# Kernel tuning notes

Measured on AMD Instinct MI355X. Metric: run time of the kernel, lower is better.

Reference implementation:

```python
import jax, jax.numpy as jnp
import numpy as np

EPS = 1e-5

def bn_relu(y, g, b):
    # BatchNorm1d in training mode: stats over (B, L) per channel, biased variance
    mu = jnp.mean(y, axis=(0, 2), keepdims=True)
    var = jnp.var(y, axis=(0, 2), keepdims=True)
    yn = (y - mu) * jax.lax.rsqrt(var + EPS)
    return jax.nn.relu(yn * g[None, :, None] + b[None, :, None])

def conv1x1_pad1(x, W):
    # Conv1d(k=1, padding=1, bias=False): pointwise matmul then zero-pad length by 1 each side
    y = jnp.einsum('bcl,oc->bol', x, W)
    return jnp.pad(y, ((0, 0), (0, 0), (1, 1)))

def conv1x1(x, W, b):
    return jnp.einsum('bcl,oc->bol', x, W) + b[None, :, None]

def conv3_pad1(x, W):
    # Conv1d(k=3, padding=1, bias=False); W: [O, C, 3]
    return jax.lax.conv_general_dilated(x, W, window_strides=(1,), padding=((1, 1),),
                                        dimension_numbers=('NCH', 'OIH', 'NCH'))

def pam(f, Wq, bq, Wk, bk, Wv, bv, gamma):
    q = conv1x1(f, Wq, bq)          # [B, C//8, L]
    k = conv1x1(f, Wk, bk)          # [B, C//8, L]
    v = conv1x1(f, Wv, bv)          # [B, C, L]
    energy = jnp.einsum('bql,bqm->blm', q, k)   # [B, L, L]
    attn = jax.nn.softmax(energy, axis=-1)
    out = jnp.einsum('bcm,blm->bcl', v, attn)
    return gamma * out + f

def cam(f, gamma):
    energy = jnp.einsum('bcl,bdl->bcd', f, f)    # [B, C, C]
    energy_new = jnp.max(energy, axis=-1, keepdims=True) - energy
    attn = jax.nn.softmax(energy_new, axis=-1)
    out = jnp.einsum('bcd,bdl->bcl', attn, f)
    return gamma * out + f

def setup_inputs() -> dict:
    key = jax.random.key(0)
    ks = jax.random.split(key, 24)
    B, C, L = 8, 256, 2046
    IC, OC = C // 4, 128  # inter_channels=64, out_channels
    s = 0.05
    d = {
        'x':   jax.random.normal(ks[0], (B, C, L), jnp.float32),
        'W5a': jax.random.normal(ks[1], (IC, C), jnp.float32) * s,
        'g5a': jnp.ones((IC,), jnp.float32), 'b5a': jnp.zeros((IC,), jnp.float32),
        'W5c': jax.random.normal(ks[2], (IC, C), jnp.float32) * s,
        'g5c': jnp.ones((IC,), jnp.float32), 'b5c': jnp.zeros((IC,), jnp.float32),
        'Wq':  jax.random.normal(ks[3], (IC // 8, IC), jnp.float32) * s,
        'bq':  jnp.zeros((IC // 8,), jnp.float32),
        'Wk':  jax.random.normal(ks[4], (IC // 8, IC), jnp.float32) * s,
        'bk':  jnp.zeros((IC // 8,), jnp.float32),
        'Wv':  jax.random.normal(ks[5], (IC, IC), jnp.float32) * s,
        'bv':  jnp.zeros((IC,), jnp.float32),
        'gamma_pam': jnp.full((1,), 0.1, jnp.float32),
        'gamma_cam': jnp.full((1,), 0.1, jnp.float32),
        'W51': jax.random.normal(ks[6], (IC, IC, 3), jnp.float32) * s,
        'g51': jnp.ones((IC,), jnp.float32), 'b51': jnp.zeros((IC,), jnp.float32),
        'W52': jax.random.normal(ks[7], (IC, IC, 3), jnp.float32) * s,
        'g52': jnp.ones((IC,), jnp.float32), 'b52': jnp.zeros((IC,), jnp.float32),
        'W6':  jax.random.normal(ks[8], (OC, IC), jnp.float32) * s,
        'b6':  jnp.zeros((OC,), jnp.float32),
        'W7':  jax.random.normal(ks[9], (OC, IC), jnp.float32) * s,
        'b7':  jnp.zeros((OC,), jnp.float32),
        'W8':  jax.random.normal(ks[10], (OC, IC), jnp.float32) * s,
        'b8':  jnp.zeros((OC,), jnp.float32),
    }
    return d

def reference(x, W5a, g5a, b5a, W5c, g5c, b5c, Wq, bq, Wk, bk, Wv, bv,
              gamma_pam, gamma_cam, W51, g51, b51, W52, g52, b52,
              W6, b6, W7, b7, W8, b8):
    # dropout (p=0.1) treated as identity (eval mode)
    feat1 = bn_relu(conv1x1_pad1(x, W5a), g5a, b5a)          # [B, IC, L+2]
    sa_feat = pam(feat1, Wq, bq, Wk, bk, Wv, bv, gamma_pam)
    sa_conv = bn_relu(conv3_pad1(sa_feat, W51), g51, b51)
    sa_output = conv1x1(sa_conv, W6, b6)                     # [B, OC, L+2]
    feat2 = bn_relu(conv1x1_pad1(x, W5c), g5c, b5c)
    sc_feat = cam(feat2, gamma_cam)
    sc_conv = bn_relu(conv3_pad1(sc_feat, W52), g52, b52)
    sc_output = conv1x1(sc_conv, W7, b7)
    feat_sum = sa_conv + sc_conv
    sasc = conv1x1(feat_sum, W8, b8)
    # pool == 'maxpool' selects AdaptiveAvgPool1d(1) in the original (note swap)
    sasc = jnp.mean(sasc, axis=-1)                            # [B, OC]
    return (sasc, sa_output, sc_output)
```

## Files before the change

### kernel.cpp

```cpp
#include <hip/hip_runtime.h>
#include <math.h>

#define B 8
#define C 256
#define L 2046
#define LP 2048
#define IC 64
#define OC 128
#define BN_EPS 1e-5f
#define INVN (1.f / 16384.f)

#define OFF_Y1T    0u
#define OFF_Y2C    524288u
#define OFF_SAFT   1048576u
#define OFF_SCFT   1572864u
#define OFF_Y51T   2097152u
#define OFF_Y52T   2621440u
#define OFF_VB     3145728u
#define OFF_QT     3670016u
#define OFF_KT     3735552u
#define OFF_LPART  3801088u
#define OFF_EPART  3866624u
#define OFF_ATTN   4390912u
#define OFF_PART1  4423680u
#define OFF_PART2  4489216u
#define OFF_COEF1  4554752u
#define OFF_COEF2  4555008u
#define OFF_FSUM   4555264u
#define OFF_W5BF   4555776u
#define OFF_W67    4572160u
#define OFF_WT     4580352u
#define OFF_WQKV   4592640u
#define OFF_BQKV   4595200u

typedef __attribute__((ext_vector_type(8))) short bshort8;
typedef __attribute__((ext_vector_type(4))) float f32x4;

__device__ __forceinline__ unsigned short f2bf(float f) {
    union { float f; unsigned int u; } v; v.f = f;
    unsigned int r = v.u + 0x7fffu + ((v.u >> 16) & 1u);
    return (unsigned short)(r >> 16);
}
__device__ __forceinline__ float bf2f(unsigned short u) {
    union { unsigned int i; float f; } v; v.i = ((unsigned int)u) << 16;
    return v.f;
}
__device__ __forceinline__ unsigned int pk2(float a, float b) {
    return (unsigned int)f2bf(a) | ((unsigned int)f2bf(b) << 16);
}

__global__ __launch_bounds__(256) void k_wprep(
        const float* __restrict__ W5a, const float* __restrict__ W5c,
        const float* __restrict__ W6, const float* __restrict__ W7,
        const float* __restrict__ W51, const float* __restrict__ W52,
        const float* __restrict__ Wq, const float* __restrict__ Wk,
        const float* __restrict__ Wv, const float* __restrict__ bq,
        const float* __restrict__ bk, const float* __restrict__ bv,
        unsigned short* __restrict__ W5BF, unsigned short* __restrict__ W67,
        unsigned short* __restrict__ WT, unsigned short* __restrict__ WQKV,
        float* __restrict__ BQKV, float* __restrict__ FSUM) {
    int i = blockIdx.x * 256 + threadIdx.x;
    if (i < 32768) {
        int o = i >> 8, c = i & 255;
        W5BF[i] = f2bf(o < 64 ? W5a[o * 256 + c] : W5c[(o - 64) * 256 + c]);
    } else if (i < 49152) {
        int j = i - 32768; int g = j >> 13; int r = j & 8191;
        W67[j] = f2bf(g ? W7[r] : W6[r]);
    } else if (i < 73728) {
        int j = i - 49152;
        int c = j & 63, o = (j >> 6) & 63, wt = j >> 12; int w = wt / 3, t = wt % 3;
        const float* Ws = w ? W52 : W51;
        WT[j] = f2bf(Ws[(o * 64 + c) * 3 + t]);
    } else if (i < 78848) {
        int j = i - 73728; int o = j >> 6, c = j & 63;
        float v = o < 8 ? Wq[o * 64 + c] : (o < 16 ? Wk[(o - 8) * 64 + c] : Wv[(o - 16) * 64 + c]);
        WQKV[j] = f2bf(v);
    } else if (i < 78928) {
        int o = i - 78848;
        BQKV[o] = o < 8 ? bq[o] : (o < 16 ? bk[o - 8] : bv[o - 16]);
    } else if (i < 79440) {
        FSUM[i - 78928] = 0.f;
    }
}

__global__ __launch_bounds__(256) void k_conv1(const float* __restrict__ x,
        const unsigned short* __restrict__ W5BF,
        unsigned short* __restrict__ Y1T, unsigned short* __restrict__ Y2C,
        float* __restrict__ PART1) {
    __shared__ float lds_part[4][128];
    int lt = blockIdx.x, og = blockIdx.y, b = blockIdx.z;
    int w = threadIdx.x >> 6, lane = threadIdx.x & 63;
    int n = lane & 15, quad = lane >> 4;
    int lp = lt * 64 + w * 16 + n;
    int ls = lp - 1;
    bool valid = (ls >= 0) && (ls < L);
    f32x4 acc[4];
#pragma unroll
    for (int ot = 0; ot < 4; ++ot) acc[ot] = (f32x4){0.f, 0.f, 0.f, 0.f};
    for (int ck = 0; ck < 8; ++ck) {
        int c0 = ck * 32 + quad * 8;
        bshort8 xb = {};
        if (valid) {
            const float* xs = x + ((size_t)(b * C + c0)) * L + ls;
#pragma unroll
            for (int j = 0; j < 8; ++j)
                ((unsigned short*)&xb)[j] = f2bf(xs[(size_t)j * L]);
        }
#pragma unroll
        for (int ot = 0; ot < 4; ++ot) {
            bshort8 wf = *(const bshort8*)(W5BF + (size_t)(og * 64 + ot * 16 + n) * C + ck * 32 + quad * 8);
            acc[ot] = __builtin_amdgcn_mfma_f32_16x16x32_bf16(wf, xb, acc[ot], 0, 0, 0);
        }
    }
    if (og == 0) {
#pragma unroll
        for (int ot = 0; ot < 4; ++ot) {
            uint2 pv;
            pv.x = pk2(acc[ot][0], acc[ot][1]);
            pv.y = pk2(acc[ot][2], acc[ot][3]);
            *(uint2*)(Y1T + ((size_t)(b * LP + lp)) * IC + ot * 16 + quad * 4) = pv;
        }
    } else {
#pragma unroll
        for (int ot = 0; ot < 4; ++ot)
#pragma unroll
            for (int r = 0; r < 4; ++r) {
                int o = ot * 16 + quad * 4 + r;
                Y2C[((size_t)(b * IC + o)) * LP + lp] = f2bf(acc[ot][r]);
            }
    }
#pragma unroll
    for (int ot = 0; ot < 4; ++ot)
#pragma unroll
        for (int r = 0; r < 4; ++r) {
            float s = acc[ot][r], q = s * s;
#pragma unroll
            for (int msk = 1; msk < 16; msk <<= 1) {
                s += __shfl_xor(s, msk, 64);
                q += __shfl_xor(q, msk, 64);
            }
            if (n == 0) {
                int ch = ot * 16 + quad * 4 + r;
                lds_part[w][ch * 2] = s;
                lds_part[w][ch * 2 + 1] = q;
            }
        }
    __syncthreads();
    int t = threadIdx.x;
    if (t < 128) {
        float s = lds_part[0][t] + lds_part[1][t] + lds_part[2][t] + lds_part[3][t];
        PART1[(size_t)(og * 128 + t) * 256 + (b * 32 + lt)] = s;
    }
}

__global__ __launch_bounds__(256) void k_red(const float* __restrict__ PART,
        const float* __restrict__ g0, const float* __restrict__ b0,
        const float* __restrict__ g1, const float* __restrict__ b1,
        float* __restrict__ COEF) {
    int ch = blockIdx.x;
    int t = threadIdx.x;
    float s = PART[(size_t)(ch * 2) * 256 + t];
    float q = PART[(size_t)(ch * 2 + 1) * 256 + t];
    for (int off = 32; off; off >>= 1) {
        s += __shfl_down(s, off, 64);
        q += __shfl_down(q, off, 64);
    }
    __shared__ float rs[4], rq[4];
    if ((t & 63) == 0) { rs[t >> 6] = s; rq[t >> 6] = q; }
    __syncthreads();
    if (t == 0) {
        float S = rs[0] + rs[1] + rs[2] + rs[3];
        float Q = rq[0] + rq[1] + rq[2] + rq[3];
        float mu = S * INVN;
        float var = Q * INVN - mu * mu;
        float gv = ch < 64 ? g0[ch] : g1[ch - 64];
        float bv = ch < 64 ? b0[ch] : b1[ch - 64];
        float A = gv * rsqrtf(var + BN_EPS);
        COEF[ch * 2] = A;
        COEF[ch * 2 + 1] = bv - mu * A;
    }
}

__global__ __launch_bounds__(256) void k_qkv(const unsigned short* __restrict__ Y1T,
        const float* __restrict__ COEF1,
        const unsigned short* __restrict__ WQKV, const float* __restrict__ BQKV,
        unsigned short* __restrict__ QT, unsigned short* __restrict__ KT,
        unsigned short* __restrict__ VB) {
    __shared__ float cA[64], cB[64];
    int lt = blockIdx.x, b = blockIdx.y;
    int t = threadIdx.x;
    if (t < 64) { cA[t] = COEF1[t * 2]; cB[t] = COEF1[t * 2 + 1]; }
    __syncthreads();
    int w = t >> 6, lane = t & 63, n = lane & 15, quad = lane >> 4;
    int lrow = lt * 64 + w * 16 + n;
    bshort8 fb[2];
#pragma unroll
    for (int kt = 0; kt < 2; ++kt) {
        bshort8 raw = *(const bshort8*)(Y1T + ((size_t)(b * LP + lrow)) * IC + kt * 32 + quad * 8);
        bshort8 f;
#pragma unroll
        for (int j = 0; j < 8; ++j) {
            int c = kt * 32 + quad * 8 + j;
            float v = fmaf(cA[c], bf2f((unsigned short)raw[j]), cB[c]);
            v = fmaxf(v, 0.f);
            ((unsigned short*)&f)[j] = f2bf(v);
        }
        fb[kt] = f;
    }
    f32x4 acc[5];
#pragma unroll
    for (int ot = 0; ot < 5; ++ot) {
        f32x4 a = {0.f, 0.f, 0.f, 0.f};
#pragma unroll
        for (int kt = 0; kt < 2; ++kt) {
            bshort8 wf = *(const bshort8*)(WQKV + (size_t)(ot * 16 + n) * IC + kt * 32 + quad * 8);
            a = __builtin_amdgcn_mfma_f32_16x16x32_bf16(wf, fb[kt], a, 0, 0, 0);
        }
        acc[ot] = a;
    }
#pragma unroll
    for (int ot = 0; ot < 5; ++ot)
#pragma unroll
        for (int r = 0; r < 4; ++r) {
            int o = ot * 16 + quad * 4 + r;
            unsigned short bv16 = f2bf(acc[ot][r] + BQKV[o]);
            if (ot == 0) {
                if (o < 8) QT[((size_t)(b * LP + lrow)) * 8 + o] = bv16;
                else KT[((size_t)(b * LP + lrow)) * 8 + (o - 8)] = bv16;
            } else {
                VB[((size_t)(b * IC + (o - 16))) * LP + lrow] = bv16;
            }
        }
}

__global__ __launch_bounds__(256) void k_pam(
        const unsigned short* __restrict__ qT, const unsigned short* __restrict__ kT,
        const unsigned short* __restrict__ vb,
        unsigned short* __restrict__ OPART, float* __restrict__ LPART) {
    __shared__ unsigned char smem[18432];
    unsigned short* vs = (unsigned short*)smem;
    unsigned short* ps = vs + 4608;
    float* os = (float*)smem;
    int qt = blockIdx.x, ks = blockIdx.y, b = blockIdx.z;
    int l0 = qt * 64;
    int tid = threadIdx.x;
    int wq = tid >> 6, lane = tid & 63, n = lane & 15, quad = lane >> 4;
    bshort8 qa = {};
    if (quad == 0)
        qa = *(const bshort8*)(qT + ((size_t)(b * LP + l0 + wq * 16 + n)) * 8);
    f32x4 acc[4];
#pragma unroll
    for (int s = 0; s < 4; ++s) acc[s] = (f32x4){0.f, 0.f, 0.f, 0.f};
    float li[4] = {0.f, 0.f, 0.f, 0.f};
    unsigned short* pw = ps + wq * 16 * 72;

    for (int it = 0; it < 8; ++it) {
        int m0 = ks * 512 + it * 64;
        __syncthreads();
        {
            int row = tid >> 2, chn = tid & 3;
            const unsigned short* src = vb + ((size_t)(b * IC + row)) * LP + m0 + chn * 16;
            unsigned short* dstl = vs + row * 72 + chn * 16;
            *(bshort8*)dstl = *(const bshort8*)src;
            *(bshort8*)(dstl + 8) = *(const bshort8*)(src + 8);
        }
        bshort8 kb[4];
#pragma unroll
        for (int s = 0; s < 4; ++s) kb[s] = (bshort8){};
        if (quad == 0) {
#pragma unroll
            for (int s = 0; s < 4; ++s)
                kb[s] = *(const bshort8*)(kT + ((size_t)(b * LP + m0 + s * 16 + n)) * 8);
        }
        __syncthreads();
        f32x4 sc[4];
#pragma unroll
        for (int s = 0; s < 4; ++s)
            sc[s] = __builtin_amdgcn_mfma_f32_16x16x32_bf16(qa, kb[s],
                        (f32x4){0.f, 0.f, 0.f, 0.f}, 0, 0, 0);
#pragma unroll
        for (int s = 0; s < 4; ++s)
#pragma unroll
            for (int r = 0; r < 4; ++r) {
                float p = __expf(sc[s][r]);
                li[r] += p;
                pw[(quad * 4 + r) * 72 + s * 16 + n] = f2bf(p);
            }
#pragma unroll
        for (int step = 0; step < 2; ++step) {
            bshort8 pa = *(const bshort8*)(pw + n * 72 + step * 32 + quad * 8);
#pragma unroll
            for (int s = 0; s < 4; ++s) {
                bshort8 vf = *(const bshort8*)(vs + (s * 16 + n) * 72 + step * 32 + quad * 8);
                acc[s] = __builtin_amdgcn_mfma_f32_16x16x32_bf16(pa, vf, acc[s], 0, 0, 0);
            }
        }
    }
    __syncthreads();
#pragma unroll
    for (int s = 0; s < 4; ++s)
#pragma unroll
        for (int r = 0; r < 4; ++r)
            os[(s * 16 + n) * 65 + wq * 16 + quad * 4 + r] = acc[s][r];
    size_t lbase = ((size_t)((b * 32 + qt) * 4 + ks)) * 64;
#pragma unroll
    for (int r = 0; r < 4; ++r) {
        float s_ = li[r];
#pragma unroll
        for (int msk = 1; msk < 16; msk <<= 1) s_ += __shfl_xor(s_, msk, 64);
        if (n == 0) LPART[lbase + wq * 16 + quad * 4 + r] = s_;
    }
    __syncthreads();
    size_t ob = ((size_t)((b * 32 + qt) * 4 + ks)) * 4096;
    int c = tid >> 2, qc = tid & 3;
    unsigned int* od = (unsigned int*)(OPART + ob + c * 64 + qc * 16);
#pragma unroll
    for (int i = 0; i < 8; ++i)
        od[i] = pk2(os[c * 65 + qc * 16 + 2 * i], os[c * 65 + qc * 16 + 2 * i + 1]);
}

__global__ __launch_bounds__(256) void k_pam_combine(
        const unsigned short* __restrict__ OPART, const float* __restrict__ LPART,
        const unsigned short* __restrict__ Y1T, const float* __restrict__ COEF1,
        const float* __restrict__ gamma, unsigned short* __restrict__ SAFT) {
    __shared__ float dn[64];
    __shared__ float cA[64], cB[64];
    __shared__ unsigned short tile[64 * 66];
    int qt = blockIdx.x, b = blockIdx.y;
    int l0 = qt * 64;
    int t = threadIdx.x;
    if (t < 64) {
        cA[t] = COEF1[t * 2]; cB[t] = COEF1[t * 2 + 1];
        size_t lbase = ((size_t)((b * 32 + qt) * 4)) * 64;
        dn[t] = LPART[lbase + t] + LPART[lbase + 64 + t] +
                LPART[lbase + 128 + t] + LPART[lbase + 192 + t];
    }
    __syncthreads();
    int c = t >> 2, qc = t & 3;
    float O[16];
#pragma unroll
    for (int i = 0; i < 16; ++i) O[i] = 0.f;
    size_t ob = ((size_t)((b * 32 + qt) * 4)) * 4096 + c * 64 + qc * 16;
#pragma unroll
    for (int s = 0; s < 4; ++s) {
        bshort8 p0 = *(const bshort8*)(OPART + ob + (size_t)s * 4096);
        bshort8 p1 = *(const bshort8*)(OPART + ob + (size_t)s * 4096 + 8);
#pragma unroll
        for (int i = 0; i < 8; ++i) {
            O[i]     += bf2f((unsigned short)p0[i]);
            O[8 + i] += bf2f((unsigned short)p1[i]);
        }
    }
    float gm = gamma[0];
#pragma unroll
    for (int i = 0; i < 16; ++i) {
        int q = qc * 16 + i;
        unsigned short raw = Y1T[((size_t)(b * LP + l0 + q)) * IC + c];
        float f1v = fmaxf(fmaf(cA[c], bf2f(raw), cB[c]), 0.f);
        float val = fmaf(gm, O[i] / dn[q], f1v);
        tile[q * 66 + c] = f2bf(val);
    }
    __syncthreads();
    int li = t >> 2, cc = t & 3;
    unsigned int* dst = (unsigned int*)(SAFT + ((size_t)(b * LP + l0 + li)) * IC + cc * 16);
#pragma unroll
    for (int i = 0; i < 8; ++i)
        dst[i] = *(unsigned int*)(tile + li * 66 + cc * 16 + 2 * i);
}

__global__ __launch_bounds__(256) void k_gram(const unsigned short* __restrict__ Y2C,
        const float* __restrict__ COEF1, float* __restrict__ EPART) {
    __shared__ float fs[64][132];
    __shared__ float cA[64], cB[64];
    int b = blockIdx.y;
    int l0 = blockIdx.x * 128;
    int t = threadIdx.x;
    if (t < 64) { cA[t] = COEF1[(64 + t) * 2]; cB[t] = COEF1[(64 + t) * 2 + 1]; }
    __syncthreads();
    for (int i = t; i < 64 * 64; i += 256) {
        int c = i >> 6, i2 = i & 63;
        unsigned int u = *(const unsigned int*)(Y2C + ((size_t)(b * IC + c)) * LP + l0 + i2 * 2);
        float A = cA[c], Bc = cB[c];
        fs[c][i2 * 2]     = fmaxf(fmaf(A, bf2f((unsigned short)u), Bc), 0.f);
        fs[c][i2 * 2 + 1] = fmaxf(fmaf(A, bf2f((unsigned short)(u >> 16)), Bc), 0.f);
    }
    __syncthreads();
    int c = t >> 2, dg = t & 3;
    float acc[16];
#pragma unroll
    for (int i = 0; i < 16; ++i) acc[i] = 0.f;
    for (int i4 = 0; i4 < 32; ++i4) {
        const float4 fc = *reinterpret_cast<const float4*>(&fs[c][i4 * 4]);
#pragma unroll
        for (int dd = 0; dd < 16; ++dd) {
            const float4 fd = *reinterpret_cast<const float4*>(&fs[dg * 16 + dd][i4 * 4]);
            acc[dd] += fc.x * fd.x + fc.y * fd.y + fc.z * fd.z + fc.w * fd.w;
        }
    }
    size_t base = ((size_t)(b * 16 + blockIdx.x)) * 4096 + c * 64 + dg * 16;
    for (int dd = 0; dd < 16; ++dd)
        EPART[base + dd] = acc[dd];
}

__global__ __launch_bounds__(256) void k_cam_softmax(const float* __restrict__ EPART,
        float* __restrict__ attn) {
    __shared__ float e[4096];
    int b = blockIdx.x, t = threadIdx.x;
    for (int idx = t; idx < 4096; idx += 256) {
        float s = 0.f;
        for (int ch = 0; ch < 16; ++ch) s += EPART[((size_t)(b * 16 + ch)) * 4096 + idx];
        e[idx] = s;
    }
    __syncthreads();
    if (t < 64) {
        float mn = INFINITY;
        for (int d = 0; d < 64; ++d) mn = fminf(mn, e[t * 64 + d]);
        float s = 0.f;
        float* a = attn + (size_t)b * 4096 + t * 64;
        for (int d = 0; d < 64; ++d) { float p = __expf(mn - e[t * 64 + d]); a[d] = p; s += p; }
        float inv = 1.f / s;
        for (int d = 0; d < 64; ++d) a[d] *= inv;
    }
}

__global__ __launch_bounds__(256) void k_cam_apply(const float* __restrict__ attn,
        const unsigned short* __restrict__ Y2C, const float* __restrict__ COEF1,
        const float* __restrict__ gamma, unsigned short* __restrict__ SCFT) {
    __shared__ __align__(16) float as[64 * 64];
    __shared__ float cA[64], cB[64];
    __shared__ unsigned short tile[128 * 66];
    int b = blockIdx.y;
    int l0 = blockIdx.x * 128;
    int t = threadIdx.x;
    int lq = t & 127, ch = t >> 7;
    if (t < 64) { cA[t] = COEF1[(64 + t) * 2]; cB[t] = COEF1[(64 + t) * 2 + 1]; }
    for (int i = t; i < 4096; i += 256) as[i] = attn[(size_t)b * 4096 + i];
    __syncthreads();
    float acc[32];
#pragma unroll
    for (int i = 0; i < 32; ++i) acc[i] = 0.f;
    const unsigned short* fb = Y2C + (size_t)b * IC * LP + l0 + lq;
    for (int d4 = 0; d4 < 16; ++d4) {
        float fv[4];
#pragma unroll
        for (int i = 0; i < 4; ++i) {
            int d = 4 * d4 + i;
            fv[i] = fmaxf(fmaf(cA[d], bf2f(fb[(size_t)d * LP]), cB[d]), 0.f);
        }
#pragma unroll
        for (int cc = 0; cc < 32; ++cc) {
            const float4 a4 = *reinterpret_cast<const float4*>(as + (ch * 32 + cc) * 64 + d4 * 4);
            acc[cc] += a4.x * fv[0] + a4.y * fv[1] + a4.z * fv[2] + a4.w * fv[3];
        }
    }
    float gm = gamma[0];
#pragma unroll
    for (int cc = 0; cc < 32; ++cc) {
        int c = ch * 32 + cc;
        float res = fmaxf(fmaf(cA[c], bf2f(fb[(size_t)c * LP]), cB[c]), 0.f);
        tile[lq * 66 + c] = f2bf(fmaf(gm, acc[cc], res));
    }
    __syncthreads();
    int li = t >> 1, half = t & 1;
    unsigned int* dst = (unsigned int*)(SCFT + ((size_t)(b * LP + l0 + li)) * IC + half * 32);
#pragma unroll
    for (int i = 0; i < 16; ++i)
        dst[i] = *(unsigned int*)(tile + li * 66 + half * 32 + 2 * i);
}

__global__ __launch_bounds__(256) void k_conv3(const unsigned short* __restrict__ SAFT,
        const unsigned short* __restrict__ SCFT, const unsigned short* __restrict__ WTall,
        unsigned short* __restrict__ Y51T, unsigned short* __restrict__ Y52T,
        float* __restrict__ PART2) {
    __shared__ float lds_part[4][128];
    int lt = blockIdx.x, og = blockIdx.y, b = blockIdx.z;
    const unsigned short* FTsrc = og ? SCFT : SAFT;
    const unsigned short* WT = WTall + og * 12288;
    unsigned short* dst = og ? Y52T : Y51T;
    int l0 = lt * 64;
    int w = threadIdx.x >> 6, lane = threadIdx.x & 63, n = lane & 15, quad = lane >> 4;
    int lrow = l0 + w * 16 + n;
    f32x4 acc[4];
#pragma unroll
    for (int ot = 0; ot < 4; ++ot) acc[ot] = (f32x4){0.f, 0.f, 0.f, 0.f};
#pragma unroll
    for (int t3 = 0; t3 < 3; ++t3) {
        int row = lrow + t3 - 1;
        bshort8 fb[2];
#pragma unroll
        for (int kt = 0; kt < 2; ++kt) {
            if (row >= 0 && row < LP)
                fb[kt] = *(const bshort8*)(FTsrc + ((size_t)(b * LP + row)) * IC + kt * 32 + quad * 8);
            else fb[kt] = (bshort8){};
        }
#pragma unroll
        for (int ot = 0; ot < 4; ++ot)
#pragma unroll
            for (int kt = 0; kt < 2; ++kt) {
                bshort8 wf = *(const bshort8*)(WT + ((size_t)(t3 * 64 + ot * 16 + n)) * IC + kt * 32 + quad * 8);
                acc[ot] = __builtin_amdgcn_mfma_f32_16x16x32_bf16(wf, fb[kt], acc[ot], 0, 0, 0);
            }
    }
#pragma unroll
    for (int ot = 0; ot < 4; ++ot) {
        uint2 pv;
        pv.x = pk2(acc[ot][0], acc[ot][1]);
        pv.y = pk2(acc[ot][2], acc[ot][3]);
        *(uint2*)(dst + ((size_t)(b * LP + lrow)) * IC + ot * 16 + quad * 4) = pv;
    }
#pragma unroll
    for (int ot = 0; ot < 4; ++ot)
#pragma unroll
        for (int r = 0; r < 4; ++r) {
            float s = acc[ot][r], q = s * s;
#pragma unroll
            for (int msk = 1; msk < 16; msk <<= 1) {
                s += __shfl_xor(s, msk, 64);
                q += __shfl_xor(q, msk, 64);
            }
            if (n == 0) {
                int cch = ot * 16 + quad * 4 + r;
                lds_part[w][cch * 2] = s;
                lds_part[w][cch * 2 + 1] = q;
            }
        }
    __syncthreads();
    int t = threadIdx.x;
    if (t < 128) {
        float s = lds_part[0][t] + lds_part[1][t] + lds_part[2][t] + lds_part[3][t];
        PART2[(size_t)(og * 128 + t) * 256 + (b * 32 + lt)] = s;
    }
}

__global__ __launch_bounds__(256) void k_final(const unsigned short* __restrict__ Y51T,
        const unsigned short* __restrict__ Y52T, const float* __restrict__ COEF2,
        const unsigned short* __restrict__ W67,
        const float* __restrict__ b6, const float* __restrict__ b7,
        float* __restrict__ out_sa, float* __restrict__ out_sc,
        float* __restrict__ FSUM) {
    __shared__ float cA[128], cB[128];
    __shared__ float fsw[4][64];
    int lt = blockIdx.x, og = blockIdx.y, b = blockIdx.z;
    int t = threadIdx.x;
    if (t < 128) { cA[t] = COEF2[t * 2]; cB[t] = COEF2[t * 2 + 1]; }
    __syncthreads();
    int w = t >> 6, lane = t & 63, n = lane & 15, quad = lane >> 4;
    int lrow = lt * 64 + w * 16 + n;
    float fs_lane[16];
    bshort8 ba[2], bb[2];
#pragma unroll
    for (int kt = 0; kt < 2; ++kt) {
        bshort8 ra = *(const bshort8*)(Y51T + ((size_t)(b * LP + lrow)) * IC + kt * 32 + quad * 8);
        bshort8 rb = *(const bshort8*)(Y52T + ((size_t)(b * LP + lrow)) * IC + kt * 32 + quad * 8);
        bshort8 fa, fb;
#pragma unroll
        for (int j = 0; j < 8; ++j) {
            int c = kt * 32 + quad * 8 + j;
            float v1 = fmaxf(fmaf(cA[c], bf2f((unsigned short)ra[j]), cB[c]), 0.f);
            float v2 = fmaxf(fmaf(cA[64 + c], bf2f((unsigned short)rb[j]), cB[64 + c]), 0.f);
            ((unsigned short*)&fa)[j] = f2bf(v1);
            ((unsigned short*)&fb)[j] = f2bf(v2);
            fs_lane[kt * 8 + j] = v1 + v2;
        }
        ba[kt] = fa; bb[kt] = fb;
    }
    f32x4 accA[4], accB[4];
#pragma unroll
    for (int ot = 0; ot < 4; ++ot) {
        accA[ot] = (f32x4){0.f, 0.f, 0.f, 0.f};
        accB[ot] = (f32x4){0.f, 0.f, 0.f, 0.f};
    }
#pragma unroll
    for (int ot = 0; ot < 4; ++ot)
#pragma unroll
        for (int kt = 0; kt < 2; ++kt) {
            bshort8 wa = *(const bshort8*)(W67 + (size_t)(og * 64 + ot * 16 + n) * IC + kt * 32 + quad * 8);
            bshort8 wb = *(const bshort8*)(W67 + 8192 + (size_t)(og * 64 + ot * 16 + n) * IC + kt * 32 + quad * 8);
            accA[ot] = __builtin_amdgcn_mfma_f32_16x16x32_bf16(wa, ba[kt], accA[ot], 0, 0, 0);
            accB[ot] = __builtin_amdgcn_mfma_f32_16x16x32_bf16(wb, bb[kt], accB[ot], 0, 0, 0);
        }
#pragma unroll
    for (int ot = 0; ot < 4; ++ot)
#pragma unroll
        for (int r = 0; r < 4; ++r) {
            int o = og * 64 + ot * 16 + quad * 4 + r;
            out_sa[((size_t)(b * OC + o)) * LP + lrow] = accA[ot][r] + b6[o];
            out_sc[((size_t)(b * OC + o)) * LP + lrow] = accB[ot][r] + b7[o];
        }
    if (og == 0) {
#pragma unroll
        for (int i = 0; i < 16; ++i) {
            float s = fs_lane[i];
#pragma unroll
            for (int msk = 1; msk < 16; msk <<= 1) s += __shfl_xor(s, msk, 64);
            if (n == 0) {
                int c = (i >> 3) * 32 + quad * 8 + (i & 7);
                fsw[w][c] = s;
            }
        }
        __syncthreads();
        if (t < 64)
            atomicAdd(&FSUM[b * 64 + t], fsw[0][t] + fsw[1][t] + fsw[2][t] + fsw[3][t]);
    }
}

__global__ __launch_bounds__(128) void k_sasc(const float* __restrict__ FSUM,
        const float* __restrict__ W8, const float* __restrict__ b8,
        float* __restrict__ out) {
    __shared__ float mean[64];
    int b = blockIdx.x, t = threadIdx.x;
    if (t < 64) mean[t] = FSUM[b * 64 + t] * (1.f / (float)LP);
    __syncthreads();
    float s = b8[t];
    for (int c = 0; c < 64; ++c) s = fmaf(W8[t * 64 + c], mean[c], s);
    out[b * OC + t] = s;
}

extern "C" void kernel_launch(void* const* d_in, const int* in_sizes, int n_in,
                              void* d_out, int out_size, void* d_ws, size_t ws_size,
                              hipStream_t stream) {
    (void)in_sizes; (void)n_in; (void)out_size; (void)ws_size;
    const float* x    = (const float*)d_in[0];
    const float* W5a  = (const float*)d_in[1];
    const float* g5a  = (const float*)d_in[2];
    const float* b5a  = (const float*)d_in[3];
    const float* W5c  = (const float*)d_in[4];
    const float* g5c  = (const float*)d_in[5];
    const float* b5c  = (const float*)d_in[6];
    const float* Wq   = (const float*)d_in[7];
    const float* bq   = (const float*)d_in[8];
    const float* Wk   = (const float*)d_in[9];
    const float* bk   = (const float*)d_in[10];
    const float* Wv   = (const float*)d_in[11];
    const float* bv   = (const float*)d_in[12];
    const float* gpam = (const float*)d_in[13];
    const float* gcam = (const float*)d_in[14];
    const float* W51  = (const float*)d_in[15];
    const float* g51  = (const float*)d_in[16];
    const float* b51  = (const float*)d_in[17];
    const float* W52  = (const float*)d_in[18];
    const float* g52  = (const float*)d_in[19];
    const float* b52  = (const float*)d_in[20];
    const float* W6   = (const float*)d_in[21];
    const float* b6   = (const float*)d_in[22];
    const float* W7   = (const float*)d_in[23];
    const float* b7   = (const float*)d_in[24];
    const float* W8   = (const float*)d_in[25];
    const float* b8   = (const float*)d_in[26];

    float* ws = (float*)d_ws;
    float* out = (float*)d_out;
    unsigned short* Y1T  = (unsigned short*)(ws + OFF_Y1T);
    unsigned short* Y2C  = (unsigned short*)(ws + OFF_Y2C);
    unsigned short* SAFT = (unsigned short*)(ws + OFF_SAFT);
    unsigned short* SCFT = (unsigned short*)(ws + OFF_SCFT);
    unsigned short* Y51T = (unsigned short*)(ws + OFF_Y51T);
    unsigned short* Y52T = (unsigned short*)(ws + OFF_Y52T);
    unsigned short* VB   = (unsigned short*)(ws + OFF_VB);
    unsigned short* QT   = (unsigned short*)(ws + OFF_QT);
    unsigned short* KT   = (unsigned short*)(ws + OFF_KT);
    float* LPART  = ws + OFF_LPART;
    float* EPART  = ws + OFF_EPART;
    float* ATTN   = ws + OFF_ATTN;
    float* PART1  = ws + OFF_PART1;
    float* PART2  = ws + OFF_PART2;
    float* COEF1  = ws + OFF_COEF1;
    float* COEF2  = ws + OFF_COEF2;
    float* FSUM   = ws + OFF_FSUM;
    unsigned short* W5BF = (unsigned short*)(ws + OFF_W5BF);
    unsigned short* W67  = (unsigned short*)(ws + OFF_W67);
    unsigned short* WT   = (unsigned short*)(ws + OFF_WT);
    unsigned short* WQKV = (unsigned short*)(ws + OFF_WQKV);
    float* BQKV = ws + OFF_BQKV;

    float* out_sa = out + B * OC;
    float* out_sc = out + B * OC + (size_t)B * OC * LP;
    unsigned short* OPART = (unsigned short*)out_sa;

    k_wprep<<<311, 256, 0, stream>>>(W5a, W5c, W6, W7, W51, W52, Wq, Wk, Wv,
                                     bq, bk, bv, W5BF, W67, WT, WQKV, BQKV, FSUM);
    k_conv1<<<dim3(32, 2, B), 256, 0, stream>>>(x, W5BF, Y1T, Y2C, PART1);
    k_red<<<128, 256, 0, stream>>>(PART1, g5a, b5a, g5c, b5c, COEF1);
    k_qkv<<<dim3(32, B), 256, 0, stream>>>(Y1T, COEF1, WQKV, BQKV, QT, KT, VB);
    k_pam<<<dim3(32, 4, B), 256, 0, stream>>>(QT, KT, VB, OPART, LPART);
    k_pam_combine<<<dim3(32, B), 256, 0, stream>>>(OPART, LPART, Y1T, COEF1, gpam, SAFT);
    k_gram<<<dim3(16, B), 256, 0, stream>>>(Y2C, COEF1, EPART);
    k_cam_softmax<<<B, 256, 0, stream>>>(EPART, ATTN);
    k_cam_apply<<<dim3(16, B), 256, 0, stream>>>(ATTN, Y2C, COEF1, gcam, SCFT);
    k_conv3<<<dim3(32, 2, B), 256, 0, stream>>>(SAFT, SCFT, WT, Y51T, Y52T, PART2);
    k_red<<<128, 256, 0, stream>>>(PART2, g51, b51, g52, b52, COEF2);
    k_final<<<dim3(32, 2, B), 256, 0, stream>>>(Y51T, Y52T, COEF2, W67, b6, b7,
                                                out_sa, out_sc, FSUM);
    k_sasc<<<B, 128, 0, stream>>>(FSUM, W8, b8, out);
}
```

Measured before the change: 243.4 us.

## Merge conv1 output groups per block and move CAM gram to bf16 MFMA

k_conv1 now computes all 128 output channels (both branches) in one block, loading and converting each x tile to bf16 once instead of twice. The launch grid halves and each block does twice the MFMA work. k_gram replaces the fp32 LDS dot-product loop with bf16 MFMA, producing 64 per-wave partial gram matrices per batch that k_cam_softmax then sums, so the workspace offsets grow. This lowers gram compute cost and x reads, but lowers gram precision to bf16 and raises the partial-sum traffic in the softmax kernel.

```diff
diff --git a/kernel.cpp b/kernel.cpp
--- a/kernel.cpp
+++ b/kernel.cpp
@@ -21,17 +21,17 @@
 #define OFF_KT     3735552u
 #define OFF_LPART  3801088u
 #define OFF_EPART  3866624u
-#define OFF_ATTN   4390912u
-#define OFF_PART1  4423680u
-#define OFF_PART2  4489216u
-#define OFF_COEF1  4554752u
-#define OFF_COEF2  4555008u
-#define OFF_FSUM   4555264u
-#define OFF_W5BF   4555776u
-#define OFF_W67    4572160u
-#define OFF_WT     4580352u
-#define OFF_WQKV   4592640u
-#define OFF_BQKV   4595200u
+#define OFF_ATTN   5963776u
+#define OFF_PART1  5996544u
+#define OFF_PART2  6062080u
+#define OFF_COEF1  6127616u
+#define OFF_COEF2  6127872u
+#define OFF_FSUM   6128128u
+#define OFF_W5BF   6128640u
+#define OFF_W67    6145024u
+#define OFF_WT     6153216u
+#define OFF_WQKV   6165504u
+#define OFF_BQKV   6168064u
 
 typedef __attribute__((ext_vector_type(8))) short bshort8;
 typedef __attribute__((ext_vector_type(4))) float f32x4;
@@ -87,50 +87,52 @@
         const unsigned short* __restrict__ W5BF,
         unsigned short* __restrict__ Y1T, unsigned short* __restrict__ Y2C,
         float* __restrict__ PART1) {
-    __shared__ float lds_part[4][128];
-    int lt = blockIdx.x, og = blockIdx.y, b = blockIdx.z;
+    __shared__ float lds_part[4][256];
+    int lt = blockIdx.x, b = blockIdx.y;
     int w = threadIdx.x >> 6, lane = threadIdx.x & 63;
     int n = lane & 15, quad = lane >> 4;
     int lp = lt * 64 + w * 16 + n;
     int ls = lp - 1;
     bool valid = (ls >= 0) && (ls < L);
-    f32x4 acc[4];
-#pragma unroll
-    for (int ot = 0; ot < 4; ++ot) acc[ot] = (f32x4){0.f, 0.f, 0.f, 0.f};
+    bshort8 xb[8];
+#pragma unroll
     for (int ck = 0; ck < 8; ++ck) {
-        int c0 = ck * 32 + quad * 8;
-        bshort8 xb = {};
+        bshort8 v = {};
         if (valid) {
-            const float* xs = x + ((size_t)(b * C + c0)) * L + ls;
+            const float* xs = x + ((size_t)(b * C + ck * 32 + quad * 8)) * L + ls;
 #pragma unroll
             for (int j = 0; j < 8; ++j)
-                ((unsigned short*)&xb)[j] = f2bf(xs[(size_t)j * L]);
-        }
-#pragma unroll
-        for (int ot = 0; ot < 4; ++ot) {
-            bshort8 wf = *(const bshort8*)(W5BF + (size_t)(og * 64 + ot * 16 + n) * C + ck * 32 + quad * 8);
-            acc[ot] = __builtin_amdgcn_mfma_f32_16x16x32_bf16(wf, xb, acc[ot], 0, 0, 0);
-        }
-    }
-    if (og == 0) {
-#pragma unroll
-        for (int ot = 0; ot < 4; ++ot) {
-            uint2 pv;
-            pv.x = pk2(acc[ot][0], acc[ot][1]);
-            pv.y = pk2(acc[ot][2], acc[ot][3]);
-            *(uint2*)(Y1T + ((size_t)(b * LP + lp)) * IC + ot * 16 + quad * 4) = pv;
-        }
-    } else {
-#pragma unroll
-        for (int ot = 0; ot < 4; ++ot)
-#pragma unroll
-            for (int r = 0; r < 4; ++r) {
-                int o = ot * 16 + quad * 4 + r;
-                Y2C[((size_t)(b * IC + o)) * LP + lp] = f2bf(acc[ot][r]);
-            }
-    }
-#pragma unroll
-    for (int ot = 0; ot < 4; ++ot)
+                ((unsigned short*)&v)[j] = f2bf(xs[(size_t)j * L]);
+        }
+        xb[ck] = v;
+    }
+    f32x4 acc[8];
+#pragma unroll
+    for (int ot = 0; ot < 8; ++ot) {
+        f32x4 a = {0.f, 0.f, 0.f, 0.f};
+#pragma unroll
+        for (int ck = 0; ck < 8; ++ck) {
+            bshort8 wf = *(const bshort8*)(W5BF + (size_t)(ot * 16 + n) * C + ck * 32 + quad * 8);
+            a = __builtin_amdgcn_mfma_f32_16x16x32_bf16(wf, xb[ck], a, 0, 0, 0);
+        }
+        acc[ot] = a;
+    }
+#pragma unroll
+    for (int ot = 0; ot < 4; ++ot) {
+        uint2 pv;
+        pv.x = pk2(acc[ot][0], acc[ot][1]);
+        pv.y = pk2(acc[ot][2], acc[ot][3]);
+        *(uint2*)(Y1T + ((size_t)(b * LP + lp)) * IC + ot * 16 + quad * 4) = pv;
+    }
+#pragma unroll
+    for (int ot = 4; ot < 8; ++ot)
+#pragma unroll
+        for (int r = 0; r < 4; ++r) {
+            int o = (ot - 4) * 16 + quad * 4 + r;
+            Y2C[((size_t)(b * IC + o)) * LP + lp] = f2bf(acc[ot][r]);
+        }
+#pragma unroll
+    for (int ot = 0; ot < 8; ++ot)
 #pragma unroll
         for (int r = 0; r < 4; ++r) {
             float s = acc[ot][r], q = s * s;
@@ -147,10 +149,8 @@
         }
     __syncthreads();
     int t = threadIdx.x;
-    if (t < 128) {
-        float s = lds_part[0][t] + lds_part[1][t] + lds_part[2][t] + lds_part[3][t];
-        PART1[(size_t)(og * 128 + t) * 256 + (b * 32 + lt)] = s;
-    }
+    float s = lds_part[0][t] + lds_part[1][t] + lds_part[2][t] + lds_part[3][t];
+    PART1[(size_t)t * 256 + (b * 32 + lt)] = s;
 }
 
 __global__ __launch_bounds__(256) void k_red(const float* __restrict__ PART,
@@ -370,36 +370,40 @@
 
 __global__ __launch_bounds__(256) void k_gram(const unsigned short* __restrict__ Y2C,
         const float* __restrict__ COEF1, float* __restrict__ EPART) {
-    __shared__ float fs[64][132];
     __shared__ float cA[64], cB[64];
-    int b = blockIdx.y;
-    int l0 = blockIdx.x * 128;
+    int blk = blockIdx.x, b = blockIdx.y;
     int t = threadIdx.x;
     if (t < 64) { cA[t] = COEF1[(64 + t) * 2]; cB[t] = COEF1[(64 + t) * 2 + 1]; }
     __syncthreads();
-    for (int i = t; i < 64 * 64; i += 256) {
-        int c = i >> 6, i2 = i & 63;
-        unsigned int u = *(const unsigned int*)(Y2C + ((size_t)(b * IC + c)) * LP + l0 + i2 * 2);
+    int w = t >> 6, lane = t & 63, n = lane & 15, quad = lane >> 4;
+    int lb = blk * 128 + w * 32 + quad * 8;
+    bshort8 frag[4];
+#pragma unroll
+    for (int g = 0; g < 4; ++g) {
+        int c = g * 16 + n;
+        bshort8 raw = *(const bshort8*)(Y2C + ((size_t)(b * IC + c)) * LP + lb);
+        bshort8 f;
         float A = cA[c], Bc = cB[c];
-        fs[c][i2 * 2]     = fmaxf(fmaf(A, bf2f((unsigned short)u), Bc), 0.f);
-        fs[c][i2 * 2 + 1] = fmaxf(fmaf(A, bf2f((unsigned short)(u >> 16)), Bc), 0.f);
-    }
-    __syncthreads();
-    int c = t >> 2, dg = t & 3;
-    float acc[16];
-#pragma unroll
-    for (int i = 0; i < 16; ++i) acc[i] = 0.f;
-    for (int i4 = 0; i4 < 32; ++i4) {
-        const float4 fc = *reinterpret_cast<const float4*>(&fs[c][i4 * 4]);
-#pragma unroll
-        for (int dd = 0; dd < 16; ++dd) {
-            const float4 fd = *reinterpret_cast<const float4*>(&fs[dg * 16 + dd][i4 * 4]);
-            acc[dd] += fc.x * fd.x + fc.y * fd.y + fc.z * fd.z + fc.w * fd.w;
-        }
-    }
-    size_t base = ((size_t)(b * 16 + blockIdx.x)) * 4096 + c * 64 + dg * 16;
-    for (int dd = 0; dd < 16; ++dd)
-        EPART[base + dd] = acc[dd];
+#pragma unroll
+        for (int j = 0; j < 8; ++j)
+            ((unsigned short*)&f)[j] = f2bf(fmaxf(fmaf(A, bf2f((unsigned short)raw[j]), Bc), 0.f));
+        frag[g] = f;
+    }
+    f32x4 acc[4][4];
+#pragma unroll
+    for (int ti = 0; ti < 4; ++ti)
+#pragma unroll
+        for (int tj = 0; tj < 4; ++tj)
+            acc[ti][tj] = __builtin_amdgcn_mfma_f32_16x16x32_bf16(frag[ti], frag[tj],
+                              (f32x4){0.f, 0.f, 0.f, 0.f}, 0, 0, 0);
+    float* ep = EPART + ((size_t)(b * 64 + blk * 4 + w)) * 4096;
+#pragma unroll
+    for (int ti = 0; ti < 4; ++ti)
+#pragma unroll
+        for (int tj = 0; tj < 4; ++tj)
+#pragma unroll
+            for (int r = 0; r < 4; ++r)
+                ep[(ti * 16 + quad * 4 + r) * 64 + tj * 16 + n] = acc[ti][tj][r];
 }
 
 __global__ __launch_bounds__(256) void k_cam_softmax(const float* __restrict__ EPART,
@@ -408,7 +412,7 @@
     int b = blockIdx.x, t = threadIdx.x;
     for (int idx = t; idx < 4096; idx += 256) {
         float s = 0.f;
-        for (int ch = 0; ch < 16; ++ch) s += EPART[((size_t)(b * 16 + ch)) * 4096 + idx];
+        for (int ch = 0; ch < 64; ++ch) s += EPART[((size_t)(b * 64 + ch)) * 4096 + idx];
         e[idx] = s;
     }
     __syncthreads();
@@ -679,7 +683,7 @@
 
     k_wprep<<<311, 256, 0, stream>>>(W5a, W5c, W6, W7, W51, W52, Wq, Wk, Wv,
                                      bq, bk, bv, W5BF, W67, WT, WQKV, BQKV, FSUM);
-    k_conv1<<<dim3(32, 2, B), 256, 0, stream>>>(x, W5BF, Y1T, Y2C, PART1);
+    k_conv1<<<dim3(32, B), 256, 0, stream>>>(x, W5BF, Y1T, Y2C, PART1);
     k_red<<<128, 256, 0, stream>>>(PART1, g5a, b5a, g5c, b5c, COEF1);
     k_qkv<<<dim3(32, B), 256, 0, stream>>>(Y1T, COEF1, WQKV, BQKV, QT, KT, VB);
     k_pam<<<dim3(32, 4, B), 256, 0, stream>>>(QT, KT, VB, OPART, LPART);
```

New measurement: 260.0 us. +6.8%, slower.
